# Kernel optimization log

Measured on AMD Instinct MI355X. Metric: run time of the kernel, lower is better.

## Reference

```python
import jax, jax.numpy as jnp
import numpy as np

N_NODES = 50000
IN_CH = 128
HID_CH = 128   # 2 * out_channels
OUT_CH = 64
N_EDGES = 800000


def setup_inputs() -> dict:
    key = jax.random.key(0)
    k1, k2, k3, k4 = jax.random.split(key, 4)
    x = jax.random.normal(k1, (N_NODES, IN_CH), dtype=jnp.float32)
    edge_index = jax.random.randint(k2, (2, N_EDGES), 0, N_NODES, dtype=jnp.int64)
    # Glorot-ish init for weights
    W1 = jax.random.normal(k3, (IN_CH, HID_CH), dtype=jnp.float32) * (1.0 / np.sqrt(IN_CH))
    b1 = jnp.zeros((HID_CH,), dtype=jnp.float32)
    W2 = jax.random.normal(k4, (HID_CH, OUT_CH), dtype=jnp.float32) * (1.0 / np.sqrt(HID_CH))
    b2 = jnp.zeros((OUT_CH,), dtype=jnp.float32)
    return {"x": x, "edge_index": edge_index, "W1": W1, "b1": b1, "W2": W2, "b2": b2}


def _gcn_norm(edge_index, num_nodes):
    """Add self-loops and compute symmetric normalization coeffs (PyG GCNConv default)."""
    loops = jnp.arange(num_nodes, dtype=edge_index.dtype)
    src = jnp.concatenate([edge_index[0], loops])  # [E + N]
    dst = jnp.concatenate([edge_index[1], loops])
    ones = jnp.ones_like(dst, dtype=jnp.float32)
    deg = jax.ops.segment_sum(ones, dst, num_segments=num_nodes)  # in-degree incl self-loop
    dinv = jnp.where(deg > 0, jax.lax.rsqrt(deg), 0.0)
    norm = dinv[src] * dinv[dst]  # [E + N]
    return src, dst, norm


def _gcn_conv(x, src, dst, norm, W, b, num_nodes):
    h = x @ W                                        # dense transform [N, d_out]
    msg = h[src] * norm[:, None]                     # gather + scale  [E+N, d_out]
    out = jax.ops.segment_sum(msg, dst, num_segments=num_nodes)  # scatter-add
    return out + b


def reference(x, edge_index, W1, b1, W2, b2):
    n = x.shape[0]
    src, dst, norm = _gcn_norm(edge_index, n)
    h = _gcn_conv(x, src, dst, norm, W1, b1, n)
    h = jax.nn.relu(h)
    out = _gcn_conv(h, src, dst, norm, W2, b2, n)
    return out
```

## Files before the change

kernel.cpp:

```cpp
#include <hip/hip_runtime.h>
#include <hip/hip_fp16.h>
#include <math.h>

#define IN_CH 128
#define CAP 64

__global__ __launch_bounds__(256) void k_build(
    const int* __restrict__ src, const int* __restrict__ dst,
    int* __restrict__ deg, int* __restrict__ slot, int E) {
    int base = (int)blockIdx.x * 2048 + (int)threadIdx.x;
    int es[8], ed[8], er[8];
    bool ev[8];
#pragma unroll
    for (int k = 0; k < 8; ++k) {
        int e = base + k * 256;
        ev[k] = (e < E);
        ed[k] = ev[k] ? dst[e] : 0;
        es[k] = ev[k] ? src[e] : 0;
    }
#pragma unroll
    for (int k = 0; k < 8; ++k) er[k] = ev[k] ? atomicAdd(&deg[ed[k]], 1) : CAP;
#pragma unroll
    for (int k = 0; k < 8; ++k) {
        if (er[k] < CAP) slot[(size_t)ed[k] * CAP + er[k]] = es[k];
    }
}

__global__ __launch_bounds__(256, 4) void k_gemm128(
    const float* __restrict__ x, const float* __restrict__ W1,
    __half* __restrict__ g1, int N) {
    constexpr int KC = 32;
    constexpr int AP = KC + 4;
    constexpr int NOUT = 128;
    constexpr int TCG = NOUT / 8;
    constexpr int BST = KC * 8 + 4;
    constexpr int TM = 4;
    __shared__ float As[64 * AP];
    __shared__ float Bs[TCG * BST];
    int tid = threadIdx.x;
    int row0 = blockIdx.x * 64;
    int cg = tid % TCG;
    int rg = tid / TCG;
    int r0 = rg * TM;

    float acc[TM][8];
#pragma unroll
    for (int r = 0; r < TM; ++r)
#pragma unroll
        for (int c = 0; c < 8; ++c) acc[r][c] = 0.f;

    for (int kc0 = 0; kc0 < IN_CH; kc0 += KC) {
        if (kc0 > 0) __syncthreads();
        for (int idx = tid; idx < 64 * (KC / 4); idx += 256) {
            int r = idx >> 3;
            int c4 = (idx & 7) * 4;
            float4 v = make_float4(0.f, 0.f, 0.f, 0.f);
            if (row0 + r < N) v = *(const float4*)(x + (size_t)(row0 + r) * IN_CH + kc0 + c4);
            *(float4*)(As + r * AP + c4) = v;
        }
        for (int idx = tid; idx < KC * (NOUT / 4); idx += 256) {
            int kk = idx / (NOUT / 4);
            int col = (idx % (NOUT / 4)) * 4;
            int cgw = col >> 3;
            int j = col & 7;
            *(float4*)(Bs + cgw * BST + kk * 8 + j) = *(const float4*)(W1 + (size_t)(kc0 + kk) * NOUT + col);
        }
        __syncthreads();

        for (int k = 0; k < KC; k += 4) {
            float4 a4[TM];
#pragma unroll
            for (int r = 0; r < TM; ++r) a4[r] = *(const float4*)(As + (r0 + r) * AP + k);
#pragma unroll
            for (int kk = 0; kk < 4; ++kk) {
                float4 b0 = *(const float4*)(Bs + cg * BST + (k + kk) * 8);
                float4 b1 = *(const float4*)(Bs + cg * BST + (k + kk) * 8 + 4);
#pragma unroll
                for (int r = 0; r < TM; ++r) {
                    float a = (kk == 0) ? a4[r].x : (kk == 1) ? a4[r].y : (kk == 2) ? a4[r].z : a4[r].w;
                    acc[r][0] += a * b0.x;
                    acc[r][1] += a * b0.y;
                    acc[r][2] += a * b0.z;
                    acc[r][3] += a * b0.w;
                    acc[r][4] += a * b1.x;
                    acc[r][5] += a * b1.y;
                    acc[r][6] += a * b1.z;
                    acc[r][7] += a * b1.w;
                }
            }
        }
    }

#pragma unroll
    for (int r = 0; r < TM; ++r) {
        int row = row0 + r0 + r;
        if (row < N) {
            union { __half2 h[4]; uint4 u; } cv;
            cv.h[0] = __floats2half2_rn(acc[r][0], acc[r][1]);
            cv.h[1] = __floats2half2_rn(acc[r][2], acc[r][3]);
            cv.h[2] = __floats2half2_rn(acc[r][4], acc[r][5]);
            cv.h[3] = __floats2half2_rn(acc[r][6], acc[r][7]);
            *(uint4*)(g1 + (size_t)row * NOUT + cg * 8) = cv.u;
        }
    }
}


__global__ __launch_bounds__(256, 4) void k_gemm64(
    const __half* __restrict__ A, const float* __restrict__ W,
    const int* __restrict__ deg, __half* __restrict__ G, int M) {
    constexpr int KC = 32;
    constexpr int AP = KC + 4;
    constexpr int NOUT = 64;
    constexpr int TCG = NOUT / 8;
    constexpr int BST = KC * 8 + 4;
    constexpr int TM = 2;
    __shared__ float As[64 * AP];
    __shared__ float Bs[TCG * BST];
    int tid = threadIdx.x;
    int row0 = blockIdx.x * 64;
    int cg = tid % TCG;
    int rg = tid / TCG;
    int r0 = rg * TM;

    float acc[TM][8];
#pragma unroll
    for (int r = 0; r < TM; ++r)
#pragma unroll
        for (int c = 0; c < 8; ++c) acc[r][c] = 0.f;

    for (int kc0 = 0; kc0 < IN_CH; kc0 += KC) {
        if (kc0 > 0) __syncthreads();
        {
            int r = tid >> 2;
            int grp = tid & 3;
            float f[8];
            if (row0 + r < M) {
                uint4 raw = *(const uint4*)(A + (size_t)(row0 + r) * IN_CH + kc0 + grp * 8);
                const __half2* h2 = (const __half2*)&raw;
#pragma unroll
                for (int q = 0; q < 4; ++q) {
                    float2 fv = __half22float2(h2[q]);
                    f[2 * q] = fv.x;
                    f[2 * q + 1] = fv.y;
                }
            } else {
#pragma unroll
                for (int q = 0; q < 8; ++q) f[q] = 0.f;
            }
            *(float4*)(As + r * AP + grp * 8) = make_float4(f[0], f[1], f[2], f[3]);
            *(float4*)(As + r * AP + grp * 8 + 4) = make_float4(f[4], f[5], f[6], f[7]);
        }
        for (int idx = tid; idx < KC * (NOUT / 4); idx += 256) {
            int kk = idx / (NOUT / 4);
            int col = (idx % (NOUT / 4)) * 4;
            int cgw = col >> 3;
            int j = col & 7;
            *(float4*)(Bs + cgw * BST + kk * 8 + j) = *(const float4*)(W + (size_t)(kc0 + kk) * NOUT + col);
        }
        __syncthreads();

        for (int k = 0; k < KC; k += 4) {
            float4 a4[TM];
#pragma unroll
            for (int r = 0; r < TM; ++r) a4[r] = *(const float4*)(As + (r0 + r) * AP + k);
#pragma unroll
            for (int kk = 0; kk < 4; ++kk) {
                float4 b0 = *(const float4*)(Bs + cg * BST + (k + kk) * 8);
                float4 b1 = *(const float4*)(Bs + cg * BST + (k + kk) * 8 + 4);
#pragma unroll
                for (int r = 0; r < TM; ++r) {
                    float a = (kk == 0) ? a4[r].x : (kk == 1) ? a4[r].y : (kk == 2) ? a4[r].z : a4[r].w;
                    acc[r][0] += a * b0.x;
                    acc[r][1] += a * b0.y;
                    acc[r][2] += a * b0.z;
                    acc[r][3] += a * b0.w;
                    acc[r][4] += a * b1.x;
                    acc[r][5] += a * b1.y;
                    acc[r][6] += a * b1.z;
                    acc[r][7] += a * b1.w;
                }
            }
        }
    }

#pragma unroll
    for (int r = 0; r < TM; ++r) {
        int row = row0 + r0 + r;
        if (row < M) {
            float d = rsqrtf((float)(deg[row] + 1));
            union { __half2 h[4]; uint4 u; } cv;
            cv.h[0] = __floats2half2_rn(d * acc[r][0], d * acc[r][1]);
            cv.h[1] = __floats2half2_rn(d * acc[r][2], d * acc[r][3]);
            cv.h[2] = __floats2half2_rn(d * acc[r][4], d * acc[r][5]);
            cv.h[3] = __floats2half2_rn(d * acc[r][6], d * acc[r][7]);
            *(uint4*)(G + (size_t)row * NOUT + cg * 8) = cv.u;
        }
    }
}


__global__ __launch_bounds__(256) void k_agg128(
    const __half* __restrict__ g, const int* __restrict__ deg, const int* __restrict__ slot,
    const float* __restrict__ bias, __half* __restrict__ out, int N) {
    int wave = threadIdx.x >> 6, lane = threadIdx.x & 63;
    int i = blockIdx.x * 4 + wave;
    if (i >= N) return;
    const __half2* gp = (const __half2*)g;
    int degi = deg[i];
    int m = min(degi, CAP);
    float dinv_i = rsqrtf((float)(degi + 1));
    float2 self = __half22float2(gp[(size_t)i * 64 + lane]);
    float2 acc = make_float2(dinv_i * self.x, dinv_i * self.y);
    const int* sl = slot + (size_t)i * CAP;
    int r = 0;
    for (; r + 8 <= m; r += 8) {
        int s[8];
#pragma unroll
        for (int j = 0; j < 8; ++j) s[j] = sl[r + j];
        __half2 v[8];
#pragma unroll
        for (int j = 0; j < 8; ++j) v[j] = gp[(size_t)s[j] * 64 + lane];
        float ds[8];
#pragma unroll
        for (int j = 0; j < 8; ++j) ds[j] = rsqrtf((float)(deg[s[j]] + 1));
#pragma unroll
        for (int j = 0; j < 8; ++j) {
            float2 f = __half22float2(v[j]);
            acc.x += ds[j] * f.x;
            acc.y += ds[j] * f.y;
        }
    }
    for (; r < m; ++r) {
        int s = sl[r];
        float dsv = rsqrtf((float)(deg[s] + 1));
        float2 f = __half22float2(gp[(size_t)s * 64 + lane]);
        acc.x += dsv * f.x;
        acc.y += dsv * f.y;
    }
    float2 b = ((const float2*)bias)[lane];
    float ox = fmaxf(dinv_i * acc.x + b.x, 0.f);
    float oy = fmaxf(dinv_i * acc.y + b.y, 0.f);
    ((__half2*)out)[(size_t)i * 64 + lane] = __floats2half2_rn(ox, oy);
}

__global__ __launch_bounds__(256) void k_agg64(
    const __half* __restrict__ g, const int* __restrict__ deg, const int* __restrict__ slot,
    const float* __restrict__ bias, float* __restrict__ out, int N) {
    int wave = threadIdx.x >> 6, lane = threadIdx.x & 63;
    int i = blockIdx.x * 4 + wave;
    if (i >= N) return;
    int degi = deg[i];
    int m = min(degi, CAP);
    float dinv_i = rsqrtf((float)(degi + 1));
    float acc = __half2float(g[(size_t)i * 64 + lane]);
    const int* sl = slot + (size_t)i * CAP;
    int r = 0;
    for (; r + 8 <= m; r += 8) {
        int s[8];
#pragma unroll
        for (int j = 0; j < 8; ++j) s[j] = sl[r + j];
        __half v[8];
#pragma unroll
        for (int j = 0; j < 8; ++j) v[j] = g[(size_t)s[j] * 64 + lane];
#pragma unroll
        for (int j = 0; j < 8; ++j) acc += __half2float(v[j]);
    }
    for (; r < m; ++r) acc += __half2float(g[(size_t)sl[r] * 64 + lane]);
    out[(size_t)i * 64 + lane] = dinv_i * acc + bias[lane];
}


static inline size_t align256(size_t x) { return (x + 255) & ~(size_t)255; }

extern "C" void kernel_launch(void* const* d_in, const int* in_sizes, int n_in,
                              void* d_out, int out_size, void* d_ws, size_t ws_size,
                              hipStream_t stream) {
    const float* x = (const float*)d_in[0];
    const int* ei = (const int*)d_in[1];
    const float* W1 = (const float*)d_in[2];
    const float* b1 = (const float*)d_in[3];
    const float* W2 = (const float*)d_in[4];
    const float* b2 = (const float*)d_in[5];
    float* out = (float*)d_out;

    const int N = in_sizes[0] / IN_CH;
    const int E = in_sizes[1] / 2;
    const int* src = ei;
    const int* dst = ei + E;

    char* p = (char*)d_ws;
    int* deg = (int*)p;       p += align256((size_t)N * 4);
    int* slot = (int*)p;      p += align256((size_t)N * CAP * 4);
    __half* g1 = (__half*)p;  p += align256((size_t)N * 128 * 2);
    __half* a1 = (__half*)p;  p += align256((size_t)N * 128 * 2);
    __half* g2 = g1;

    const int GB = (N + 63) / 64;
    const int BB = (E + 2047) / 2048;

    hipMemsetAsync(deg, 0, (size_t)N * 4, stream);
    k_build<<<BB, 256, 0, stream>>>(src, dst, deg, slot, E);
    k_gemm128<<<GB, 256, 0, stream>>>(x, W1, g1, N);
    k_agg128<<<(N + 3) / 4, 256, 0, stream>>>(g1, deg, slot, b1, a1, N);
    k_gemm64<<<GB, 256, 0, stream>>>(a1, W2, deg, g2, N);
    k_agg64<<<(N + 3) / 4, 256, 0, stream>>>(g2, deg, slot, b2, out, N);
}
```

Before: 243.9 us.

## Fuse graph build with first GEMM, narrow slot indices, precompute dinv

Merges the edge-bucketing kernel and the first dense GEMM into one launch, where the first BB blocks build the adjacency and the rest compute x@W1, so the two independent stages can overlap. Slot indices shrink from int to unsigned short, halving CSR storage and gather-index traffic. Normalisation factors are precomputed into a dinv array by a new small kernel, replacing a per-neighbour deg load plus rsqrt with a single float load. The 16-bit indices only hold while N is at most 65536, and the extra launch adds a little overhead.

```diff
diff --git a/kernel.cpp b/kernel.cpp
--- a/kernel.cpp
+++ b/kernel.cpp
@@ -5,30 +5,12 @@
 #define IN_CH 128
 #define CAP 64
 
-__global__ __launch_bounds__(256) void k_build(
+
+__global__ __launch_bounds__(256, 4) void k_gemm_build(
+    const float* __restrict__ x, const float* __restrict__ W1,
+    __half* __restrict__ g1, int N,
     const int* __restrict__ src, const int* __restrict__ dst,
-    int* __restrict__ deg, int* __restrict__ slot, int E) {
-    int base = (int)blockIdx.x * 2048 + (int)threadIdx.x;
-    int es[8], ed[8], er[8];
-    bool ev[8];
-#pragma unroll
-    for (int k = 0; k < 8; ++k) {
-        int e = base + k * 256;
-        ev[k] = (e < E);
-        ed[k] = ev[k] ? dst[e] : 0;
-        es[k] = ev[k] ? src[e] : 0;
-    }
-#pragma unroll
-    for (int k = 0; k < 8; ++k) er[k] = ev[k] ? atomicAdd(&deg[ed[k]], 1) : CAP;
-#pragma unroll
-    for (int k = 0; k < 8; ++k) {
-        if (er[k] < CAP) slot[(size_t)ed[k] * CAP + er[k]] = es[k];
-    }
-}
-
-__global__ __launch_bounds__(256, 4) void k_gemm128(
-    const float* __restrict__ x, const float* __restrict__ W1,
-    __half* __restrict__ g1, int N) {
+    int* __restrict__ deg, unsigned short* __restrict__ slot, int E, int BB) {
     constexpr int KC = 32;
     constexpr int AP = KC + 4;
     constexpr int NOUT = 128;
@@ -38,7 +20,28 @@
     __shared__ float As[64 * AP];
     __shared__ float Bs[TCG * BST];
     int tid = threadIdx.x;
-    int row0 = blockIdx.x * 64;
+
+    if ((int)blockIdx.x < BB) {
+        int base = (int)blockIdx.x * 2048 + tid;
+        int es[8], ed[8], er[8];
+        bool ev[8];
+#pragma unroll
+        for (int k = 0; k < 8; ++k) {
+            int e = base + k * 256;
+            ev[k] = (e < E);
+            ed[k] = ev[k] ? dst[e] : 0;
+            es[k] = ev[k] ? src[e] : 0;
+        }
+#pragma unroll
+        for (int k = 0; k < 8; ++k) er[k] = ev[k] ? atomicAdd(&deg[ed[k]], 1) : CAP;
+#pragma unroll
+        for (int k = 0; k < 8; ++k) {
+            if (er[k] < CAP) slot[(size_t)ed[k] * CAP + er[k]] = (unsigned short)es[k];
+        }
+        return;
+    }
+
+    int row0 = ((int)blockIdx.x - BB) * 64;
     int cg = tid % TCG;
     int rg = tid / TCG;
     int r0 = rg * TM;
@@ -105,10 +108,16 @@
     }
 }
 
+__global__ __launch_bounds__(256) void k_dinv(
+    const int* __restrict__ deg, float* __restrict__ dinv, int N) {
+    int i = blockIdx.x * 256 + threadIdx.x;
+    if (i < N) dinv[i] = rsqrtf((float)(deg[i] + 1));
+}
+
 
 __global__ __launch_bounds__(256, 4) void k_gemm64(
     const __half* __restrict__ A, const float* __restrict__ W,
-    const int* __restrict__ deg, __half* __restrict__ G, int M) {
+    const float* __restrict__ dinv, __half* __restrict__ G, int M) {
     constexpr int KC = 32;
     constexpr int AP = KC + 4;
     constexpr int NOUT = 64;
@@ -188,7 +197,7 @@
     for (int r = 0; r < TM; ++r) {
         int row = row0 + r0 + r;
         if (row < M) {
-            float d = rsqrtf((float)(deg[row] + 1));
+            float d = dinv[row];
             union { __half2 h[4]; uint4 u; } cv;
             cv.h[0] = __floats2half2_rn(d * acc[r][0], d * acc[r][1]);
             cv.h[1] = __floats2half2_rn(d * acc[r][2], d * acc[r][3]);
@@ -201,18 +210,19 @@
 
 
 __global__ __launch_bounds__(256) void k_agg128(
-    const __half* __restrict__ g, const int* __restrict__ deg, const int* __restrict__ slot,
-    const float* __restrict__ bias, __half* __restrict__ out, int N) {
+    const __half* __restrict__ g, const float* __restrict__ dinv,
+    const unsigned short* __restrict__ slot,
+    const float* __restrict__ bias, __half* __restrict__ out, int N,
+    const int* __restrict__ deg) {
     int wave = threadIdx.x >> 6, lane = threadIdx.x & 63;
     int i = blockIdx.x * 4 + wave;
     if (i >= N) return;
     const __half2* gp = (const __half2*)g;
-    int degi = deg[i];
-    int m = min(degi, CAP);
-    float dinv_i = rsqrtf((float)(degi + 1));
+    int m = min(deg[i], CAP);
+    float dinv_i = dinv[i];
     float2 self = __half22float2(gp[(size_t)i * 64 + lane]);
     float2 acc = make_float2(dinv_i * self.x, dinv_i * self.y);
-    const int* sl = slot + (size_t)i * CAP;
+    const unsigned short* sl = slot + (size_t)i * CAP;
     int r = 0;
     for (; r + 8 <= m; r += 8) {
         int s[8];
@@ -223,7 +233,7 @@
         for (int j = 0; j < 8; ++j) v[j] = gp[(size_t)s[j] * 64 + lane];
         float ds[8];
 #pragma unroll
-        for (int j = 0; j < 8; ++j) ds[j] = rsqrtf((float)(deg[s[j]] + 1));
+        for (int j = 0; j < 8; ++j) ds[j] = dinv[s[j]];
 #pragma unroll
         for (int j = 0; j < 8; ++j) {
             float2 f = __half22float2(v[j]);
@@ -233,7 +243,7 @@
     }
     for (; r < m; ++r) {
         int s = sl[r];
-        float dsv = rsqrtf((float)(deg[s] + 1));
+        float dsv = dinv[s];
         float2 f = __half22float2(gp[(size_t)s * 64 + lane]);
         acc.x += dsv * f.x;
         acc.y += dsv * f.y;
@@ -245,16 +255,17 @@
 }
 
 __global__ __launch_bounds__(256) void k_agg64(
-    const __half* __restrict__ g, const int* __restrict__ deg, const int* __restrict__ slot,
-    const float* __restrict__ bias, float* __restrict__ out, int N) {
+    const __half* __restrict__ g, const float* __restrict__ dinv,
+    const unsigned short* __restrict__ slot,
+    const float* __restrict__ bias, float* __restrict__ out, int N,
+    const int* __restrict__ deg) {
     int wave = threadIdx.x >> 6, lane = threadIdx.x & 63;
     int i = blockIdx.x * 4 + wave;
     if (i >= N) return;
-    int degi = deg[i];
-    int m = min(degi, CAP);
-    float dinv_i = rsqrtf((float)(degi + 1));
+    int m = min(deg[i], CAP);
+    float dinv_i = dinv[i];
     float acc = __half2float(g[(size_t)i * 64 + lane]);
-    const int* sl = slot + (size_t)i * CAP;
+    const unsigned short* sl = slot + (size_t)i * CAP;
     int r = 0;
     for (; r + 8 <= m; r += 8) {
         int s[8];
@@ -290,19 +301,20 @@
     const int* dst = ei + E;
 
     char* p = (char*)d_ws;
-    int* deg = (int*)p;       p += align256((size_t)N * 4);
-    int* slot = (int*)p;      p += align256((size_t)N * CAP * 4);
-    __half* g1 = (__half*)p;  p += align256((size_t)N * 128 * 2);
-    __half* a1 = (__half*)p;  p += align256((size_t)N * 128 * 2);
+    int* deg = (int*)p;                 p += align256((size_t)N * 4);
+    float* dinv = (float*)p;            p += align256((size_t)N * 4);
+    unsigned short* slot = (unsigned short*)p;  p += align256((size_t)N * CAP * 2);
+    __half* g1 = (__half*)p;            p += align256((size_t)N * 128 * 2);
+    __half* a1 = (__half*)p;            p += align256((size_t)N * 128 * 2);
     __half* g2 = g1;
 
     const int GB = (N + 63) / 64;
     const int BB = (E + 2047) / 2048;
 
     hipMemsetAsync(deg, 0, (size_t)N * 4, stream);
-    k_build<<<BB, 256, 0, stream>>>(src, dst, deg, slot, E);
-    k_gemm128<<<GB, 256, 0, stream>>>(x, W1, g1, N);
-    k_agg128<<<(N + 3) / 4, 256, 0, stream>>>(g1, deg, slot, b1, a1, N);
-    k_gemm64<<<GB, 256, 0, stream>>>(a1, W2, deg, g2, N);
-    k_agg64<<<(N + 3) / 4, 256, 0, stream>>>(g2, deg, slot, b2, out, N);
-}
+    k_gemm_build<<<BB + GB, 256, 0, stream>>>(x, W1, g1, N, src, dst, deg, slot, E, BB);
+    k_dinv<<<(N + 255) / 256, 256, 0, stream>>>(deg, dinv, N);
+    k_agg128<<<(N + 3) / 4, 256, 0, stream>>>(g1, dinv, slot, b1, a1, N, deg);
+    k_gemm64<<<GB, 256, 0, stream>>>(a1, W2, dinv, g2, N);
+    k_agg64<<<(N + 3) / 4, 256, 0, stream>>>(g2, dinv, slot, b2, out, N, deg);
+}
```

Measured after the change: 231.0 us. 1.06x faster.
